# Kernel tuning notes

Measured on AMD Instinct MI355X. Metric: run time of the kernel, lower is better.

Reference implementation:

```python
import jax, jax.numpy as jnp
import numpy as np


def setup_inputs() -> dict:
    key = jax.random.key(0)
    k1, k2, k3 = jax.random.split(key, 3)
    x = jax.random.normal(k1, (32, 256, 32, 32), dtype=jnp.float32)
    weight = jax.random.normal(k2, (256, 256, 3, 3), dtype=jnp.float32) * 0.05
    bias = jax.random.normal(k3, (256,), dtype=jnp.float32) * 0.01
    return {"x": x, "weight": weight, "bias": bias}


def _forward(x, weight, bias):
    B, cin, n, _ = x.shape
    cout, _, k, _ = weight.shape
    s = (k - 1) // 2
    nf = n // 2 + 1
    bins = n * nf

    # fft shift matrix: exp(-1j*2*pi*s*(i+j)/n), kept rfft columns
    idx = jnp.arange(n)
    shift = idx[None, :] + idx[:, None]                     # (n, n)
    shift_m = jnp.exp(-1j * 2 * jnp.pi * s * shift / n)[:, :nf]
    shift_m = shift_m.reshape(bins, 1, 1).astype(jnp.complex64)

    # xfft: (B, cin, n, nf) -> (bins, cin, B)
    xfft = jnp.fft.rfft2(x)
    xfft = jnp.transpose(xfft, (2, 3, 1, 0)).reshape(bins, cin, B)

    # Hfft: (cout, cin, n, nf) -> (bins, cout, cin), shifted + conj
    Hfft = jnp.fft.rfft2(weight, s=(n, n)).reshape(cout, cin, bins)
    Hfft = shift_m * jnp.conj(jnp.transpose(Hfft, (2, 0, 1)))

    def sq_abs(z):
        return jnp.real(z) ** 2 + jnp.imag(z) ** 2

    RowNorm = jnp.sqrt(jnp.sum(sq_abs(Hfft), axis=2))       # (bins, cout)
    ColNorm = jnp.sqrt(jnp.sum(sq_abs(Hfft), axis=1))       # (bins, cin)

    if cout >= cin:
        RowLoss = jnp.mean((RowNorm - jnp.sqrt(cin / cout)) ** 2)
        ColLoss = jnp.mean((ColNorm - 1.0) ** 2)
        HHT = jnp.einsum('npc,nqc->npq', jnp.conj(Hfft), Hfft)  # (bins, cout, cout)
        mask = jnp.triu(jnp.ones((cout, cout), bool), k=1)
        count = bins * (cout * (cout - 1) // 2)
        AngLoss = jnp.sum(sq_abs(HHT) * mask[None]) / count   # MSE(|HHT[triu]|, 0)
        L = cout * ColLoss + cin * RowLoss + AngLoss
    else:
        RowLoss = jnp.mean((RowNorm - 1.0) ** 2)
        ColLoss = jnp.mean((ColNorm - jnp.sqrt(cout / cin)) ** 2)
        HTH = jnp.einsum('ndp,ndq->npq', jnp.conj(Hfft), Hfft)  # (bins, cin, cin)
        mask = jnp.triu(jnp.ones((cin, cin), bool), k=1)
        count = bins * (cin * (cin - 1) // 2)
        AngLoss = jnp.sum(sq_abs(HTH) * mask[None]) / count
        L = cout * ColLoss + cin * RowLoss + AngLoss

    # per-bin complex matmul: (bins, cout, cin) @ (bins, cin, B) -> (bins, cout, B)
    yfft = Hfft @ xfft
    yfft = jnp.transpose(yfft.reshape(n, nf, cout, B), (3, 2, 0, 1))  # (B, cout, n, nf)
    y = jnp.fft.irfft2(yfft, s=(n, n))
    y = y + bias[None, :, None, None]
    return y, L


def reference(x, weight, bias):
    return _forward(x, weight, bias)
```

## Files before the change

### kernel.cpp

```cpp
#include <hip/hip_runtime.h>
#include <math.h>

typedef __attribute__((ext_vector_type(8)))  short  short8;
typedef __attribute__((ext_vector_type(16))) float  float16;

#define TWO_PI_OVER_32 0.19634954084936207f

static __device__ __forceinline__ unsigned short f2bf(float f) {
    unsigned int u = __float_as_uint(f);
    u = (u + 0x7FFFu + ((u >> 16) & 1u)) >> 16;
    return (unsigned short)u;
}
static __device__ __forceinline__ float bf2f(unsigned short s) {
    return __uint_as_float(((unsigned int)s) << 16);
}

static __device__ __forceinline__ void g2l16(const void* g, void* l) {
    __builtin_amdgcn_global_load_lds(
        (const __attribute__((address_space(1))) unsigned int*)g,
        (__attribute__((address_space(3))) unsigned int*)l, 16, 0, 0);
}

#define WAITV(n) do { asm volatile("s_waitcnt vmcnt(" #n ")" ::: "memory"); \
                      __builtin_amdgcn_sched_barrier(0); } while (0)

__global__ __launch_bounds__(256) void k_prepx(const float* __restrict__ x,
                                               unsigned short* __restrict__ xb,
                                               const float* __restrict__ w,
                                               unsigned short* __restrict__ wt,
                                               unsigned short* __restrict__ Vb,
                                               float* __restrict__ Drow,
                                               float* __restrict__ Dcol) {
    __shared__ union {
        unsigned short tr[8 * 1024];
        struct { float sdata[45]; float ws2[256 * 9]; } wm;
    } sh;
    int tid = threadIdx.x;

    if (blockIdx.x < 1024) {
        int b = blockIdx.x >> 5, cig = blockIdx.x & 31;
        int r = tid >> 3, c4 = (tid & 7) * 4;
        const float4* xv = (const float4*)(x + ((size_t)(b * 256 + cig * 8)) * 1024);
        #pragma unroll
        for (int u = 0; u < 8; ++u) {
            float4 v = xv[u * 256 + r * 8 + (c4 >> 2)];
            union { unsigned short s[4]; uint2 d; } pk;
            pk.s[0] = f2bf(v.x); pk.s[1] = f2bf(v.y);
            pk.s[2] = f2bf(v.z); pk.s[3] = f2bf(v.w);
            *(uint2*)&sh.tr[u * 1024 + r * 32 + c4] = pk.d;
        }
        __syncthreads();
        uint4* dst = (uint4*)xb + ((size_t)b * 32 + cig) * 1024;
        #pragma unroll
        for (int k = 0; k < 4; ++k) {
            int g = tid * 4 + k;
            union { unsigned short u[8]; uint4 v; } pk;
            #pragma unroll
            for (int u = 0; u < 8; ++u) pk.u[u] = sh.tr[u * 1024 + g];
            dst[g] = pk.v;
        }
        return;
    }

    int blk = blockIdx.x - 1024, lane = tid & 63;
    bool colmode = blk >= 256;
    int pc = blk & 255;
    if (tid < 45) sh.wm.sdata[tid] = 0.f;

    int p = colmode ? tid : pc;
    int c = colmode ? pc : tid;
    float w9[9];
    #pragma unroll
    for (int t = 0; t < 9; ++t) w9[t] = w[(p * 256 + c) * 9 + t];
    if (!colmode) {
        #pragma unroll
        for (int t = 0; t < 9; ++t) sh.wm.ws2[tid * 9 + t] = w9[t];
    }
    __syncthreads();

    int idx = 0;
    for (int ta = 0; ta < 9; ++ta)
        for (int tb = ta; tb < 9; ++tb) {
            float v = w9[ta] * w9[tb];
            #pragma unroll
            for (int off = 32; off > 0; off >>= 1) v += __shfl_down(v, off);
            if (lane == 0) atomicAdd(&sh.wm.sdata[idx], v);
            ++idx;
        }
    __syncthreads();
    if (tid < 45) (colmode ? Dcol : Drow)[tid * 256 + pc] = sh.wm.sdata[tid];

    if (!colmode) {
        #pragma unroll
        for (int t = 0; t < 9; ++t)
            wt[t * 65536 + (c >> 3) * 2048 + p * 8 + (c & 7)] = f2bf(w9[t]);
        if (tid < 320) {
            int ta = tid >> 5, cig = tid & 31;
            union { unsigned short u[8]; uint4 v; } pk;
            #pragma unroll
            for (int u = 0; u < 8; ++u)
                pk.u[u] = (ta < 9) ? f2bf(sh.wm.ws2[(cig * 8 + u) * 9 + ta]) : (unsigned short)0;
            ((uint4*)Vb)[(p * 10 + ta) * 32 + cig] = pk.v;
        }
    }
}

__global__ __launch_bounds__(64, 2) void k_conv(const unsigned short* __restrict__ xb,
                                                const unsigned short* __restrict__ wt,
                                                const float* __restrict__ bias,
                                                const unsigned short* __restrict__ Vb,
                                                unsigned short* __restrict__ Gb,
                                                float* __restrict__ y) {
    __shared__ unsigned short xs[2][640 * 8];
    __shared__ unsigned short wsm[2][576 * 8];

    const int lane = threadIdx.x & 63;
    const int half = lane >> 5;
    const int m    = lane & 31;

    if (blockIdx.x >= 1024) {
        int blk = blockIdx.x - 1024, I = 0;
        while (blk >= 40 - I) { blk -= 40 - I; ++I; }
        int J = I + blk;
        const int row0 = I * 64;
        const int col0 = J * 64;

        float16 acc[2][2];
        #pragma unroll
        for (int i = 0; i < 2; ++i)
            #pragma unroll
            for (int j = 0; j < 2; ++j)
                #pragma unroll
                for (int r = 0; r < 16; ++r) acc[i][j][r] = 0.f;

        const short8* vb = (const short8*)Vb;
        for (int kc = 0; kc < 16; ++kc) {
            int cig = kc * 2 + half;
            short8 a0 = vb[(row0 + m) * 32 + cig];
            short8 a1 = vb[(row0 + 32 + m) * 32 + cig];
            short8 b0 = vb[(col0 + m) * 32 + cig];
            short8 b1 = vb[(col0 + 32 + m) * 32 + cig];
            acc[0][0] = __builtin_amdgcn_mfma_f32_32x32x16_bf16(a0, b0, acc[0][0], 0, 0, 0);
            acc[0][1] = __builtin_amdgcn_mfma_f32_32x32x16_bf16(a0, b1, acc[0][1], 0, 0, 0);
            acc[1][0] = __builtin_amdgcn_mfma_f32_32x32x16_bf16(a1, b0, acc[1][0], 0, 0, 0);
            acc[1][1] = __builtin_amdgcn_mfma_f32_32x32x16_bf16(a1, b1, acc[1][1], 0, 0, 0);
        }
        #pragma unroll
        for (int i = 0; i < 2; ++i)
            #pragma unroll
            for (int j = 0; j < 2; ++j)
                #pragma unroll
                for (int reg = 0; reg < 16; ++reg) {
                    int crow = (reg & 3) + 8 * (reg >> 2) + 4 * half;
                    Gb[(row0 + i * 32 + crow) * 2560 + col0 + j * 32 + m] =
                        f2bf(acc[i][j][reg]);
                }
        return;
    }

    const int id    = blockIdx.x;
    const int xcd   = id & 7;
    const int local = id >> 3;
    const int b     = xcd * 4 + (local >> 5);
    const int rem   = local & 31;
    const int co0   = (rem & 7) * 32;
    const int r0    = (rem >> 3) * 8;

    float16 acc[8];
    #pragma unroll
    for (int ns = 0; ns < 8; ++ns)
        #pragma unroll
        for (int r = 0; r < 16; ++r) acc[ns][r] = 0.f;

    const uint4* xbv = (const uint4*)xb;
    const uint4* wtv = (const uint4*)wt;

    const int cigl = lane >> 5;
    const int coll = lane & 31;

    auto stage_x = [&](int buf, int kc) {
        uint4* xd = (uint4*)xs[buf];
        #pragma unroll
        for (int ch = 0; ch < 10; ++ch) {
            int gr = (r0 + ch + 31) & 31;
            g2l16(&xbv[((b * 32 + kc * 2 + cigl) * 32 + gr) * 32 + coll],
                  &xd[ch * 64]);
        }
    };
    auto stage_w = [&](int buf, int kc) {
        uint4* wd = (uint4*)wsm[buf];
        #pragma unroll
        for (int t = 0; t < 9; ++t) {
            g2l16(&wtv[t * 8192 + (kc * 2 + cigl) * 256 + co0 + coll],
                  &wd[t * 64]);
        }
    };

    auto compute = [&](int buf) {
        const short8* xsl = (const short8*)xs[buf];
        const short8* wsl = (const short8*)wsm[buf];
        #pragma unroll
        for (int btv = 0; btv < 3; ++btv) {
            int gc = (m + btv + 31) & 31;
            short8 bfr[10];
            #pragma unroll
            for (int sl = 0; sl < 10; ++sl)
                bfr[sl] = xsl[(sl * 2 + half) * 32 + gc];
            #pragma unroll
            for (int atv = 0; atv < 3; ++atv) {
                int t = atv * 3 + btv;
                short8 a = wsl[(t * 2 + half) * 32 + m];
                #pragma unroll
                for (int ns = 0; ns < 8; ++ns) {
                    acc[ns] = __builtin_amdgcn_mfma_f32_32x32x16_bf16(
                        a, bfr[ns + atv], acc[ns], 0, 0, 0);
                }
            }
        }
    };

    stage_w(0, 0);
    stage_x(0, 0);
    #pragma unroll 1
    for (int kc = 0; kc < 16; ++kc) {
        int buf = kc & 1;
        if (kc < 15) {
            stage_w(buf ^ 1, kc + 1);
            stage_x(buf ^ 1, kc + 1);
            WAITV(19);
        } else {
            WAITV(0);
        }
        __builtin_amdgcn_s_setprio(1);
        compute(buf);
        __builtin_amdgcn_s_setprio(0);
    }

    #pragma unroll
    for (int ns = 0; ns < 8; ++ns) {
        int r = r0 + ns;
        #pragma unroll
        for (int reg = 0; reg < 16; ++reg) {
            int crow = (reg & 3) + 8 * (reg >> 2) + 4 * half;
            int co = co0 + crow;
            y[(b * 256 + co) * 1024 + r * 32 + m] = acc[ns][reg] + bias[co];
        }
    }
}

__global__ __launch_bounds__(256) void k_loss(const float* __restrict__ Drow,
                                              const float* __restrict__ Dcol,
                                              const unsigned short* __restrict__ Gb,
                                              float* __restrict__ rowp,
                                              float* __restrict__ colp,
                                              float* __restrict__ angp) {
    __shared__ union {
        struct { float coef[45]; float red[2]; } rc;
        struct { unsigned short gs[9 * 2560]; float red; } ang;
    } sh;
    int tid = threadIdx.x;

    if (blockIdx.x < 544) {
        int bin = blockIdx.x;
        int u = bin / 17, v = bin % 17;
        if (tid < 2) sh.rc.red[tid] = 0.f;
        if (tid < 45) {
            int idx = 0, TA = 0, TB = 0;
            for (int ta = 0; ta < 9; ++ta)
                for (int tb = ta; tb < 9; ++tb) {
                    if (idx == tid) { TA = ta; TB = tb; }
                    ++idx;
                }
            int da = TA / 3 - TB / 3;
            int db = TA % 3 - TB % 3;
            float cth = cosf(TWO_PI_OVER_32 * (float)(u * da + v * db));
            sh.rc.coef[tid] = (TA == TB) ? 1.f : 2.f * cth;
        }
        __syncthreads();

        float s1 = 0.f, s2 = 0.f;
        const float* dr = Drow + tid;
        const float* dc = Dcol + tid;
        #pragma unroll
        for (int i = 0; i < 45; ++i) {
            s1 += sh.rc.coef[i] * dr[i * 256];
            s2 += sh.rc.coef[i] * dc[i * 256];
        }
        float e1 = sqrtf(fmaxf(s1, 0.f)) - 1.f; e1 *= e1;
        float e2 = sqrtf(fmaxf(s2, 0.f)) - 1.f; e2 *= e2;
        #pragma unroll
        for (int off = 32; off > 0; off >>= 1) {
            e1 += __shfl_down(e1, off);
            e2 += __shfl_down(e2, off);
        }
        if ((tid & 63) == 0) { atomicAdd(&sh.rc.red[0], e1); atomicAdd(&sh.rc.red[1], e2); }
        __syncthreads();
        if (tid == 0) { rowp[bin] = sh.rc.red[0]; colp[bin] = sh.rc.red[1]; }
    } else {
        int p = blockIdx.x - 544;
        if (tid == 0) sh.ang.red = 0.f;
        uint4* gsv = (uint4*)sh.ang.gs;
        const uint4* gbv = (const uint4*)Gb;
        for (int i = tid; i < 2880; i += 256) {
            int rr = i / 320, cc = i - rr * 320;
            gsv[i] = gbv[(p * 10 + rr) * 320 + cc];
        }
        __syncthreads();

        int q = tid;
        float S = 0.f;
        if (q > p) {
            float g5[5][5];
            #pragma unroll
            for (int i = 0; i < 5; ++i)
                #pragma unroll
                for (int j = 0; j < 5; ++j) g5[i][j] = 0.f;
            #pragma unroll
            for (int ta = 0; ta < 9; ++ta)
                #pragma unroll
                for (int tb = 0; tb < 9; ++tb) {
                    float c = bf2f(sh.ang.gs[ta * 2560 + q * 10 + tb]);
                    g5[ta / 3 - tb / 3 + 2][ta % 3 - tb % 3 + 2] += c;
                }
            #pragma unroll
            for (int da = 0; da < 5; ++da) {
                const float* g = g5[da];
                float sq = g[0]*g[0] + g[1]*g[1] + g[2]*g[2] + g[3]*g[3] + g[4]*g[4];
                float cr = g[0]*g[2] + g[1]*g[3] + g[2]*g[4] + g[0]*g[4];
                S += 17.f * sq + 2.f * cr;
            }
            S *= 32.f;
        }
        #pragma unroll
        for (int off = 32; off > 0; off >>= 1) S += __shfl_down(S, off);
        if ((tid & 63) == 0) atomicAdd(&sh.ang.red, S);
        __syncthreads();
        if (tid == 0) angp[p] = sh.ang.red;
    }
}

__global__ __launch_bounds__(256) void k_fin(const float* __restrict__ rowp,
                                             const float* __restrict__ colp,
                                             const float* __restrict__ angp,
                                             float* __restrict__ out) {
    __shared__ float sred[3][4];
    int tid = threadIdx.x;
    float r = 0.f, c = 0.f, a = 0.f;
    for (int i = tid; i < 544; i += 256) { r += rowp[i]; c += colp[i]; }
    a = angp[tid];
    #pragma unroll
    for (int off = 32; off > 0; off >>= 1) {
        r += __shfl_down(r, off);
        c += __shfl_down(c, off);
        a += __shfl_down(a, off);
    }
    if ((tid & 63) == 0) {
        int wv = tid >> 6;
        sred[0][wv] = r; sred[1][wv] = c; sred[2][wv] = a;
    }
    __syncthreads();
    if (tid == 0) {
        float R = sred[0][0] + sred[0][1] + sred[0][2] + sred[0][3];
        float C = sred[1][0] + sred[1][1] + sred[1][2] + sred[1][3];
        float A = sred[2][0] + sred[2][1] + sred[2][2] + sred[2][3];
        out[8388608] = R / 544.f + C / 544.f + A / (544.f * 32640.f);
    }
}

extern "C" void kernel_launch(void* const* d_in, const int* in_sizes, int n_in,
                              void* d_out, int out_size, void* d_ws, size_t ws_size,
                              hipStream_t stream) {
    const float* x    = (const float*)d_in[0];
    const float* w    = (const float*)d_in[1];
    const float* bias = (const float*)d_in[2];
    float* out = (float*)d_out;

    char* ws = (char*)d_ws;
    unsigned short* wt = (unsigned short*)ws;
    unsigned short* xb = (unsigned short*)(ws + 1179648);
    unsigned short* Vb = (unsigned short*)(ws + 17956864);
    float* Drow  = (float*)(ws + 19267584);
    float* Dcol  = (float*)(ws + 19313664);
    float* rowp  = (float*)(ws + 19359744);
    float* colp  = (float*)(ws + 19361920);
    float* angp  = (float*)(ws + 19364096);
    unsigned short* Gb = (unsigned short*)(ws + 19392512);

    k_prepx <<<1536, 256, 0, stream>>>(x, xb, w, wt, Vb, Drow, Dcol);
    k_conv  <<<1844, 64, 0, stream>>>(xb, wt, bias, Vb, Gb, out);
    k_loss  <<<800, 256, 0, stream>>>(Drow, Dcol, Gb, rowp, colp, angp);
    k_fin   <<<1, 256, 0, stream>>>(rowp, colp, angp, out);
}
```

Before: 156.4 us.

## Split conv tile across two waves sharing LDS staging, single-buffer x

The conv kernel moves from one 64-thread wave per block to two waves. Each wave computes 4 of the 8 output rows and the two waves split the global-to-LDS staging of x and weights. The x tile becomes single-buffered, with barriers around compute and the next x load issued after compute, so less LDS per block lets more blocks stay resident. The Gram-tile blocks now run two tiles per block, and the prep kernel's store index is changed so consecutive threads write consecutive addresses. The cost is extra barriers, x loads no longer overlapping compute, and duplicated B-fragment reads across the waves.

```diff
diff --git a/kernel.cpp b/kernel.cpp
--- a/kernel.cpp
+++ b/kernel.cpp
@@ -21,6 +21,8 @@
         (__attribute__((address_space(3))) unsigned int*)l, 16, 0, 0);
 }
 
+#define SBAR() do { __builtin_amdgcn_s_barrier(); \
+                    __builtin_amdgcn_sched_barrier(0); } while (0)
 #define WAITV(n) do { asm volatile("s_waitcnt vmcnt(" #n ")" ::: "memory"); \
                       __builtin_amdgcn_sched_barrier(0); } while (0)
 
@@ -53,7 +55,7 @@
         uint4* dst = (uint4*)xb + ((size_t)b * 32 + cig) * 1024;
         #pragma unroll
         for (int k = 0; k < 4; ++k) {
-            int g = tid * 4 + k;
+            int g = k * 256 + tid;
             union { unsigned short u[8]; uint4 v; } pk;
             #pragma unroll
             for (int u = 0; u < 8; ++u) pk.u[u] = sh.tr[u * 1024 + g];
@@ -105,23 +107,26 @@
     }
 }
 
-__global__ __launch_bounds__(64, 2) void k_conv(const unsigned short* __restrict__ xb,
-                                                const unsigned short* __restrict__ wt,
-                                                const float* __restrict__ bias,
-                                                const unsigned short* __restrict__ Vb,
-                                                unsigned short* __restrict__ Gb,
-                                                float* __restrict__ y) {
-    __shared__ unsigned short xs[2][640 * 8];
+__global__ __launch_bounds__(128, 3) void k_conv(const unsigned short* __restrict__ xb,
+                                                 const unsigned short* __restrict__ wt,
+                                                 const float* __restrict__ bias,
+                                                 const unsigned short* __restrict__ Vb,
+                                                 unsigned short* __restrict__ Gb,
+                                                 float* __restrict__ y) {
+    __shared__ unsigned short xs[640 * 8];
     __shared__ unsigned short wsm[2][576 * 8];
 
-    const int lane = threadIdx.x & 63;
+    const int tid  = threadIdx.x;
+    const int wv   = tid >> 6;
+    const int lane = tid & 63;
     const int half = lane >> 5;
     const int m    = lane & 31;
 
     if (blockIdx.x >= 1024) {
-        int blk = blockIdx.x - 1024, I = 0;
-        while (blk >= 40 - I) { blk -= 40 - I; ++I; }
-        int J = I + blk;
+        int tile = (blockIdx.x - 1024) * 2 + wv;
+        int I = 0;
+        while (tile >= 40 - I) { tile -= 40 - I; ++I; }
+        int J = I + tile;
         const int row0 = I * 64;
         const int col0 = J * 64;
 
@@ -166,9 +171,9 @@
     const int co0   = (rem & 7) * 32;
     const int r0    = (rem >> 3) * 8;
 
-    float16 acc[8];
+    float16 acc[4];
     #pragma unroll
-    for (int ns = 0; ns < 8; ++ns)
+    for (int ns = 0; ns < 4; ++ns)
         #pragma unroll
         for (int r = 0; r < 16; ++r) acc[ns][r] = 0.f;
 
@@ -178,10 +183,10 @@
     const int cigl = lane >> 5;
     const int coll = lane & 31;
 
-    auto stage_x = [&](int buf, int kc) {
-        uint4* xd = (uint4*)xs[buf];
-        #pragma unroll
-        for (int ch = 0; ch < 10; ++ch) {
+    auto stage_x = [&](int kc) {
+        uint4* xd = (uint4*)xs;
+        #pragma unroll
+        for (int ch = wv; ch < 10; ch += 2) {
             int gr = (r0 + ch + 31) & 31;
             g2l16(&xbv[((b * 32 + kc * 2 + cigl) * 32 + gr) * 32 + coll],
                   &xd[ch * 64]);
@@ -190,55 +195,58 @@
     auto stage_w = [&](int buf, int kc) {
         uint4* wd = (uint4*)wsm[buf];
         #pragma unroll
-        for (int t = 0; t < 9; ++t) {
+        for (int t = wv; t < 9; t += 2) {
             g2l16(&wtv[t * 8192 + (kc * 2 + cigl) * 256 + co0 + coll],
                   &wd[t * 64]);
         }
     };
 
     auto compute = [&](int buf) {
-        const short8* xsl = (const short8*)xs[buf];
+        const short8* xsl = (const short8*)xs;
         const short8* wsl = (const short8*)wsm[buf];
         #pragma unroll
         for (int btv = 0; btv < 3; ++btv) {
             int gc = (m + btv + 31) & 31;
-            short8 bfr[10];
-            #pragma unroll
-            for (int sl = 0; sl < 10; ++sl)
-                bfr[sl] = xsl[(sl * 2 + half) * 32 + gc];
-            #pragma unroll
-            for (int atv = 0; atv < 3; ++atv) {
-                int t = atv * 3 + btv;
-                short8 a = wsl[(t * 2 + half) * 32 + m];
+            short8 a[3];
+            #pragma unroll
+            for (int atv = 0; atv < 3; ++atv)
+                a[atv] = wsl[((atv * 3 + btv) * 2 + half) * 32 + m];
+            #pragma unroll
+            for (int s = 0; s < 6; ++s) {
+                short8 bf = xsl[((wv * 4 + s) * 2 + half) * 32 + gc];
                 #pragma unroll
-                for (int ns = 0; ns < 8; ++ns) {
-                    acc[ns] = __builtin_amdgcn_mfma_f32_32x32x16_bf16(
-                        a, bfr[ns + atv], acc[ns], 0, 0, 0);
+                for (int atv = 0; atv < 3; ++atv) {
+                    int ns = s - atv;
+                    if (ns >= 0 && ns < 4)
+                        acc[ns] = __builtin_amdgcn_mfma_f32_32x32x16_bf16(
+                            a[atv], bf, acc[ns], 0, 0, 0);
                 }
             }
         }
     };
 
     stage_w(0, 0);
-    stage_x(0, 0);
+    stage_x(0);
     #pragma unroll 1
     for (int kc = 0; kc < 16; ++kc) {
         int buf = kc & 1;
         if (kc < 15) {
             stage_w(buf ^ 1, kc + 1);
-            stage_x(buf ^ 1, kc + 1);
-            WAITV(19);
+            if (wv == 0) { WAITV(5); } else { WAITV(4); }
         } else {
             WAITV(0);
         }
+        SBAR();
         __builtin_amdgcn_s_setprio(1);
         compute(buf);
         __builtin_amdgcn_s_setprio(0);
+        SBAR();
+        if (kc < 15) stage_x(kc + 1);
     }
 
     #pragma unroll
-    for (int ns = 0; ns < 8; ++ns) {
-        int r = r0 + ns;
+    for (int ns = 0; ns < 4; ++ns) {
+        int r = r0 + wv * 4 + ns;
         #pragma unroll
         for (int reg = 0; reg < 16; ++reg) {
             int crow = (reg & 3) + 8 * (reg >> 2) + 4 * half;
@@ -387,7 +395,7 @@
     unsigned short* Gb = (unsigned short*)(ws + 19392512);
 
     k_prepx <<<1536, 256, 0, stream>>>(x, xb, w, wt, Vb, Drow, Dcol);
-    k_conv  <<<1844, 64, 0, stream>>>(xb, wt, bias, Vb, Gb, out);
+    k_conv  <<<1434, 128, 0, stream>>>(xb, wt, bias, Vb, Gb, out);
     k_loss  <<<800, 256, 0, stream>>>(Drow, Dcol, Gb, rowp, colp, angp);
     k_fin   <<<1, 256, 0, stream>>>(rowp, colp, angp, out);
 }
```

Result: no change. 155.5 us (-0.6%).
